# Performance work log

Measured on AMD Instinct MI355X. Metric: run time of the kernel, lower is better.

## Reference

```python
import jax, jax.numpy as jnp
import numpy as np

OUT, IN, GS = 8192, 8192, 128
N_GROUPS = OUT * IN // GS  # 524288


def setup_inputs() -> dict:
    key = jax.random.key(0)
    k1, k2, k3 = jax.random.split(key, 3)
    x = jax.random.normal(k1, (32, IN), dtype=jnp.float32)
    # ternary values in {-1, 0, 1}
    ternary = jax.random.randint(k2, (OUT, IN), -1, 2, dtype=jnp.int32)
    # positive per-group scales
    scales = jax.random.uniform(k3, (N_GROUPS,), dtype=jnp.float32, minval=0.01, maxval=0.1)
    return {"x": x, "ternary": ternary, "scales": scales}


def reference(x, ternary, scales):
    # Dequantize: each contiguous group of GS weights shares one scale.
    # scales: [n_groups] -> [n_groups, GS] -> [OUT, IN]
    scales_exp = jnp.broadcast_to(scales[:, None], (N_GROUPS, GS)).reshape(OUT, IN)
    w = ternary.astype(jnp.float32) * scales_exp  # [OUT, IN]
    # F.linear(x, w) = x @ w.T
    return jnp.einsum("ti,oi->to", x, w)
```

## Files before the change

### kernel.cpp

```cpp
#include <hip/hip_runtime.h>
#include <stdint.h>

#define OUT_DIM 8192
#define IN_DIM  8192
#define GS      128
#define MROWS   32
#define NSPLIT  8
#define KCHUNK  1024
#define KS      64
#define NSTG    (KCHUNK / KS)
#define PART_ELEMS (MROWS * OUT_DIM)

typedef __attribute__((ext_vector_type(8))) short bf16x8;
typedef __attribute__((ext_vector_type(4))) float f32x4;
typedef __attribute__((ext_vector_type(8))) unsigned short u16x8;

__device__ __forceinline__ unsigned short f2bf_rne(float f) {
    uint32_t v = __builtin_bit_cast(uint32_t, f);
    v += 0x7FFFu + ((v >> 16) & 1u);
    return (unsigned short)(v >> 16);
}

__global__ __launch_bounds__(256) void prep_xbf(const float* __restrict__ x,
                                                unsigned short* __restrict__ xbf) {
    int i = (blockIdx.x * 256 + threadIdx.x) * 8;
    float4 a = *(const float4*)(x + i);
    float4 b = *(const float4*)(x + i + 4);
    float f[8] = {a.x, a.y, a.z, a.w, b.x, b.y, b.z, b.w};
    u16x8 u;
#pragma unroll
    for (int j = 0; j < 8; ++j) u[j] = f2bf_rne(f[j]);
    *(u16x8*)(xbf + i) = u;
}

__global__ __launch_bounds__(256) void ternary_gemm(
    const int* __restrict__ tern, const float* __restrict__ scales,
    const unsigned short* __restrict__ xbf, float* __restrict__ part) {
    __shared__ __align__(16) int lds_w[2][64][68];

    const int tid  = threadIdx.x;
    const int wv   = tid >> 6;
    const int lane = tid & 63;
    const int n    = lane & 15;
    const int quad = lane >> 4;

    const int otile = blockIdx.x & 127;
    const int kc    = blockIdx.x >> 7;
    const int o0    = otile << 6;
    const int o     = o0 + (wv << 4) + n;
    const int kpos0 = kc << 10;

    const int srow = tid >> 4;
    const int scol = (tid & 15) << 2;
    const int* __restrict__ wbase = tern + (size_t)o0 * IN_DIM + kpos0 + scol;

    const unsigned short* __restrict__ xr0 = xbf + n * IN_DIM + kpos0 + (quad << 3);
    const unsigned short* __restrict__ xr1 = xbf + (16 + n) * IN_DIM + kpos0 + (quad << 3);
    const float* __restrict__ sp = scales + o * (IN_DIM / GS) + (kc << 3);

    f32x4 acc0 = {0.f, 0.f, 0.f, 0.f};
    f32x4 acc1 = {0.f, 0.f, 0.f, 0.f};

    {
        int4 s0 = *(const int4*)(wbase + (size_t)srow * IN_DIM);
        int4 s1 = *(const int4*)(wbase + (size_t)(16 + srow) * IN_DIM);
        int4 s2 = *(const int4*)(wbase + (size_t)(32 + srow) * IN_DIM);
        int4 s3 = *(const int4*)(wbase + (size_t)(48 + srow) * IN_DIM);
        *(int4*)&lds_w[0][srow][scol]      = s0;
        *(int4*)&lds_w[0][16 + srow][scol] = s1;
        *(int4*)&lds_w[0][32 + srow][scol] = s2;
        *(int4*)&lds_w[0][48 + srow][scol] = s3;
    }
    __syncthreads();

    float s_nxt = sp[0];

#pragma unroll 1
    for (int stg = 0; stg < NSTG; ++stg) {
        const int buf = stg & 1;
        int4 s0, s1, s2, s3;
        if (stg < NSTG - 1) {
            const int* __restrict__ wb = wbase + (stg + 1) * KS;
            s0 = *(const int4*)(wb + (size_t)srow * IN_DIM);
            s1 = *(const int4*)(wb + (size_t)(16 + srow) * IN_DIM);
            s2 = *(const int4*)(wb + (size_t)(32 + srow) * IN_DIM);
            s3 = *(const int4*)(wb + (size_t)(48 + srow) * IN_DIM);
        }
        const float s_use  = s_nxt;
        const float s_pref = sp[(stg < NSTG - 1) ? ((stg + 1) >> 1) : 7];
        const unsigned int p = f2bf_rne(s_use);

        const int kk0  = stg * KS;
        const int lrow = (wv << 4) + n;
#pragma unroll
        for (int half = 0; half < 2; ++half) {
            const int kk = half << 5;
            int4 w0 = *(const int4*)&lds_w[buf][lrow][kk + (quad << 3)];
            int4 w1 = *(const int4*)&lds_w[buf][lrow][kk + (quad << 3) + 4];
            bf16x8 a0 = *(const bf16x8*)(xr0 + kk0 + kk);
            bf16x8 a1 = *(const bf16x8*)(xr1 + kk0 + kk);
            int tw[8] = {w0.x, w0.y, w0.z, w0.w, w1.x, w1.y, w1.z, w1.w};
            bf16x8 bfr;
#pragma unroll
            for (int j = 0; j < 8; ++j) {
                int t = tw[j];
                unsigned int v = p | ((unsigned int)t & 0x8000u);
                bfr[j] = (short)((t == 0) ? 0u : v);
            }
            acc0 = __builtin_amdgcn_mfma_f32_16x16x32_bf16(a0, bfr, acc0, 0, 0, 0);
            acc1 = __builtin_amdgcn_mfma_f32_16x16x32_bf16(a1, bfr, acc1, 0, 0, 0);
        }
        if (stg < NSTG - 1) {
            *(int4*)&lds_w[buf ^ 1][srow][scol]      = s0;
            *(int4*)&lds_w[buf ^ 1][16 + srow][scol] = s1;
            *(int4*)&lds_w[buf ^ 1][32 + srow][scol] = s2;
            *(int4*)&lds_w[buf ^ 1][48 + srow][scol] = s3;
        }
        __syncthreads();
        s_nxt = s_pref;
    }

    float* __restrict__ prow = part + (size_t)kc * PART_ELEMS;
#pragma unroll
    for (int r = 0; r < 4; ++r) {
        prow[(quad * 4 + r) * OUT_DIM + o]      = acc0[r];
        prow[(quad * 4 + r + 16) * OUT_DIM + o] = acc1[r];
    }
}

__global__ __launch_bounds__(256) void reduce_parts(const float* __restrict__ part,
                                                    float* __restrict__ out) {
    const int i = (blockIdx.x * 256 + threadIdx.x) * 4;
    float4 s = *(const float4*)(part + i);
#pragma unroll
    for (int kc = 1; kc < NSPLIT; ++kc) {
        float4 v = *(const float4*)(part + (size_t)kc * PART_ELEMS + i);
        s.x += v.x; s.y += v.y; s.z += v.z; s.w += v.w;
    }
    *(float4*)(out + i) = s;
}

extern "C" void kernel_launch(void* const* d_in, const int* in_sizes, int n_in,
                              void* d_out, int out_size, void* d_ws, size_t ws_size,
                              hipStream_t stream) {
    const float* x      = (const float*)d_in[0];
    const int*   tern   = (const int*)d_in[1];
    const float* scales = (const float*)d_in[2];
    float* out = (float*)d_out;

    unsigned short* xbf = (unsigned short*)d_ws;
    float* part = (float*)((char*)d_ws + (512 << 10));

    prep_xbf<<<128, 256, 0, stream>>>(x, xbf);
    ternary_gemm<<<128 * NSPLIT, 256, 0, stream>>>(tern, scales, xbf, part);
    reduce_parts<<<256, 256, 0, stream>>>(part, out);
}
```

Baseline: 408.5 us.

## Stage x through LDS, swizzle tiles, prefetch two stages, use packed ternary conversion

Rebuilds the main loop so activation tiles are also staged in LDS instead of being read directly from global memory by each wave. Weight and x register prefetch now runs two stages ahead into a single LDS buffer, with two barriers per stage, and an XOR swizzle on LDS columns. The per-element ternary-to-bf16 select is replaced by a byte-permute plus packed 16-bit multiply that handles two values at once. The goal is to hide global latency better and cut ALU work in the conversion, at the cost of an extra barrier per stage and more registers held live.

```diff
diff --git a/kernel.cpp b/kernel.cpp
--- a/kernel.cpp
+++ b/kernel.cpp
@@ -14,6 +14,8 @@
 typedef __attribute__((ext_vector_type(8))) short bf16x8;
 typedef __attribute__((ext_vector_type(4))) float f32x4;
 typedef __attribute__((ext_vector_type(8))) unsigned short u16x8;
+typedef __attribute__((ext_vector_type(2))) unsigned short u16x2;
+typedef __attribute__((ext_vector_type(4))) unsigned int   u32x4;
 
 __device__ __forceinline__ unsigned short f2bf_rne(float f) {
     uint32_t v = __builtin_bit_cast(uint32_t, f);
@@ -33,10 +35,30 @@
     *(u16x8*)(xbf + i) = u;
 }
 
+__device__ __forceinline__ unsigned int cvt2(int t0, int t1, unsigned int p32) {
+    unsigned int t16 = __builtin_amdgcn_perm((unsigned int)t1, (unsigned int)t0,
+                                             0x05040100u);
+    unsigned int v   = p32 | (t16 & 0x80008000u);
+    u16x2 r = __builtin_bit_cast(u16x2, v) *
+              __builtin_bit_cast(u16x2, t16 & 0x00010001u);
+    return __builtin_bit_cast(unsigned int, r);
+}
+
+__device__ __forceinline__ bf16x8 conv8(const int4 wa, const int4 wb, unsigned int p32) {
+    u32x4 d;
+    d[0] = cvt2(wa.x, wa.y, p32);
+    d[1] = cvt2(wa.z, wa.w, p32);
+    d[2] = cvt2(wb.x, wb.y, p32);
+    d[3] = cvt2(wb.z, wb.w, p32);
+    return __builtin_bit_cast(bf16x8, d);
+}
+
+#define WSW(r, c) ((c) ^ (((r) & 7) << 3))
 __global__ __launch_bounds__(256) void ternary_gemm(
     const int* __restrict__ tern, const float* __restrict__ scales,
     const unsigned short* __restrict__ xbf, float* __restrict__ part) {
-    __shared__ __align__(16) int lds_w[2][64][68];
+    __shared__ __align__(16) int            lw[64][68];
+    __shared__ __align__(16) unsigned short lx[32][72];
 
     const int tid  = threadIdx.x;
     const int wv   = tid >> 6;
@@ -54,71 +76,63 @@
     const int scol = (tid & 15) << 2;
     const int* __restrict__ wbase = tern + (size_t)o0 * IN_DIM + kpos0 + scol;
 
-    const unsigned short* __restrict__ xr0 = xbf + n * IN_DIM + kpos0 + (quad << 3);
-    const unsigned short* __restrict__ xr1 = xbf + (16 + n) * IN_DIM + kpos0 + (quad << 3);
+    const int xrow = tid >> 3;
+    const int xcol = (tid & 7) << 3;
+    const unsigned short* __restrict__ xbase =
+        xbf + (size_t)xrow * IN_DIM + kpos0 + xcol;
+
     const float* __restrict__ sp = scales + o * (IN_DIM / GS) + (kc << 3);
 
     f32x4 acc0 = {0.f, 0.f, 0.f, 0.f};
     f32x4 acc1 = {0.f, 0.f, 0.f, 0.f};
 
-    {
-        int4 s0 = *(const int4*)(wbase + (size_t)srow * IN_DIM);
-        int4 s1 = *(const int4*)(wbase + (size_t)(16 + srow) * IN_DIM);
-        int4 s2 = *(const int4*)(wbase + (size_t)(32 + srow) * IN_DIM);
-        int4 s3 = *(const int4*)(wbase + (size_t)(48 + srow) * IN_DIM);
-        *(int4*)&lds_w[0][srow][scol]      = s0;
-        *(int4*)&lds_w[0][16 + srow][scol] = s1;
-        *(int4*)&lds_w[0][32 + srow][scol] = s2;
-        *(int4*)&lds_w[0][48 + srow][scol] = s3;
-    }
+#define WLOAD(d0, d1, d2, d3, T) do { const int* wb = wbase + (T) * KS;        \
+        d0 = *(const int4*)(wb + (size_t) srow       * IN_DIM);                \
+        d1 = *(const int4*)(wb + (size_t)(srow + 16) * IN_DIM);                \
+        d2 = *(const int4*)(wb + (size_t)(srow + 32) * IN_DIM);                \
+        d3 = *(const int4*)(wb + (size_t)(srow + 48) * IN_DIM); } while (0)
+#define XLOAD(d, T) (d) = *(const bf16x8*)(xbase + (T) * KS)
+#define WWRITE(s0, s1, s2, s3) do { const int c = WSW(srow, scol);             \
+        *(int4*)&lw[srow     ][c] = s0; *(int4*)&lw[srow + 16][c] = s1;        \
+        *(int4*)&lw[srow + 32][c] = s2; *(int4*)&lw[srow + 48][c] = s3; } while (0)
+#define XWRITE(v) *(bf16x8*)&lx[xrow][WSW(xrow, xcol)] = (v)
+
+    int4 wn0, wn1, wn2, wn3; bf16x8 xn;
+    WLOAD(wn0, wn1, wn2, wn3, 0); XLOAD(xn, 0);
+    WWRITE(wn0, wn1, wn2, wn3);   XWRITE(xn);
+    WLOAD(wn0, wn1, wn2, wn3, 1); XLOAD(xn, 1);
+    int4 wf0 = wn0, wf1 = wn1, wf2 = wn2, wf3 = wn3; bf16x8 xf = xn;
     __syncthreads();
 
-    float s_nxt = sp[0];
+    const int lrow = (wv << 4) + n;
+    const int qo   = quad << 3;
 
 #pragma unroll 1
-    for (int stg = 0; stg < NSTG; ++stg) {
-        const int buf = stg & 1;
-        int4 s0, s1, s2, s3;
-        if (stg < NSTG - 1) {
-            const int* __restrict__ wb = wbase + (stg + 1) * KS;
-            s0 = *(const int4*)(wb + (size_t)srow * IN_DIM);
-            s1 = *(const int4*)(wb + (size_t)(16 + srow) * IN_DIM);
-            s2 = *(const int4*)(wb + (size_t)(32 + srow) * IN_DIM);
-            s3 = *(const int4*)(wb + (size_t)(48 + srow) * IN_DIM);
-        }
-        const float s_use  = s_nxt;
-        const float s_pref = sp[(stg < NSTG - 1) ? ((stg + 1) >> 1) : 7];
-        const unsigned int p = f2bf_rne(s_use);
-
-        const int kk0  = stg * KS;
-        const int lrow = (wv << 4) + n;
+    for (int s = 0; s < NSTG; ++s) {
+        if (s + 2 < NSTG) { WLOAD(wf0, wf1, wf2, wf3, s + 2); XLOAD(xf, s + 2); }
+        const unsigned int ph  = f2bf_rne(sp[s >> 1]);
+        const unsigned int p32 = ph | (ph << 16);
 #pragma unroll
         for (int half = 0; half < 2; ++half) {
-            const int kk = half << 5;
-            int4 w0 = *(const int4*)&lds_w[buf][lrow][kk + (quad << 3)];
-            int4 w1 = *(const int4*)&lds_w[buf][lrow][kk + (quad << 3) + 4];
-            bf16x8 a0 = *(const bf16x8*)(xr0 + kk0 + kk);
-            bf16x8 a1 = *(const bf16x8*)(xr1 + kk0 + kk);
-            int tw[8] = {w0.x, w0.y, w0.z, w0.w, w1.x, w1.y, w1.z, w1.w};
-            bf16x8 bfr;
-#pragma unroll
-            for (int j = 0; j < 8; ++j) {
-                int t = tw[j];
-                unsigned int v = p | ((unsigned int)t & 0x8000u);
-                bfr[j] = (short)((t == 0) ? 0u : v);
-            }
+            const int kk  = (half << 5) + qo;
+            const int wc  = WSW(lrow, kk);
+            int4 w0 = *(const int4*)&lw[lrow][wc];
+            int4 w1 = *(const int4*)&lw[lrow][wc + 4];
+            bf16x8 a0 = *(const bf16x8*)&lx[n     ][WSW(n, kk)];
+            bf16x8 a1 = *(const bf16x8*)&lx[16 + n][WSW(n, kk)];
+            bf16x8 bfr = conv8(w0, w1, p32);
             acc0 = __builtin_amdgcn_mfma_f32_16x16x32_bf16(a0, bfr, acc0, 0, 0, 0);
             acc1 = __builtin_amdgcn_mfma_f32_16x16x32_bf16(a1, bfr, acc1, 0, 0, 0);
         }
-        if (stg < NSTG - 1) {
-            *(int4*)&lds_w[buf ^ 1][srow][scol]      = s0;
-            *(int4*)&lds_w[buf ^ 1][16 + srow][scol] = s1;
-            *(int4*)&lds_w[buf ^ 1][32 + srow][scol] = s2;
-            *(int4*)&lds_w[buf ^ 1][48 + srow][scol] = s3;
-        }
         __syncthreads();
-        s_nxt = s_pref;
+        if (s + 1 < NSTG) { WWRITE(wn0, wn1, wn2, wn3); XWRITE(xn); }
+        __syncthreads();
+        wn0 = wf0; wn1 = wf1; wn2 = wf2; wn3 = wf3; xn = xf;
     }
+#undef WLOAD
+#undef XLOAD
+#undef WWRITE
+#undef XWRITE
 
     float* __restrict__ prow = part + (size_t)kc * PART_ELEMS;
 #pragma unroll
```

New measurement: 412.7 us. About the same (+1.0%).
